# Optimization experiments

Hardware: AMD Instinct MI355X
Metric: run time of the kernel (lower is better)

## Reference

```python
import jax, jax.numpy as jnp
import numpy as np

B, M, K, N = 4, 2048, 4096, 4096


def setup_inputs() -> dict:
    key = jax.random.key(0)
    k1, k2, k3, k4, k5 = jax.random.split(key, 5)
    # quantized activations in [-8, 7], stored as int8 (spec dtype int32, cast here)
    x_q = jax.random.randint(k1, (B, M, K), -8, 8, dtype=jnp.int32).astype(jnp.int8)
    # per-token activation scales (B, M, 1)
    scales_x = jax.random.uniform(k2, (B, M, 1), dtype=jnp.float32, minval=0.001, maxval=0.02)
    # int8 weight (N, K) in [-8, 7] as produced by from_float
    weight = jax.random.randint(k3, (N, K), -8, 8, dtype=jnp.int32).astype(jnp.int8)
    # per-output-row weight scales (N, 1)
    weight_scales = jax.random.uniform(k4, (N, 1), dtype=jnp.float32, minval=0.001, maxval=0.02)
    bias = jax.random.normal(k5, (N,), dtype=jnp.float32) * 0.02
    return {"x_q": x_q, "scales_x": scales_x, "weight": weight,
            "weight_scales": weight_scales, "bias": bias}


def reference(x_q, scales_x, weight, weight_scales, bias):
    acc = jnp.einsum('bmk,nk->bmn', x_q, weight,
                     preferred_element_type=jnp.int32)  # (B, M, N) int32
    # sym_dequant: per-token scale * per-row weight scale, then fused bias add
    out = acc.astype(jnp.float32) * scales_x * weight_scales.reshape(1, 1, N) + bias
    return out
```

## Files before the change

kernel.cpp:

```cpp
#include <hip/hip_runtime.h>
#include <stdint.h>

#define MROWS 8192
#define K_DIM 4096
#define N_DIM 4096
#define BM 128
#define BN 128
#define BK 64

#define X_ELEMS (MROWS * K_DIM)
#define W_ELEMS (N_DIM * K_DIM)

typedef __attribute__((ext_vector_type(4))) int int4v;

#define GLOAD_LDS16(gptr, lptr)                                                   \
    __builtin_amdgcn_global_load_lds((const __attribute__((address_space(1))) void*)(gptr), \
                                     (__attribute__((address_space(3))) void*)(lptr), 16, 0, 0)

__device__ __forceinline__ int pack4(int4v v) {
    return (int)((unsigned)(v[0] & 0xFF)
               | ((unsigned)(v[1] & 0xFF) << 8)
               | ((unsigned)(v[2] & 0xFF) << 16)
               | ((unsigned)(v[3] & 0xFF) << 24));
}

__global__ __launch_bounds__(256) void pack_i32_to_i8(
    const int4v* __restrict__ src, int4v* __restrict__ dst, int n16)
{
    int i = blockIdx.x * blockDim.x + threadIdx.x;
    if (i >= n16) return;
    int4v a = src[4 * i + 0];
    int4v b = src[4 * i + 1];
    int4v c = src[4 * i + 2];
    int4v d = src[4 * i + 3];
    int4v r;
    r[0] = pack4(a); r[1] = pack4(b); r[2] = pack4(c); r[3] = pack4(d);
    dst[i] = r;
}

__global__ __launch_bounds__(256) void i8gemm_dq_kernel(
    const int8_t* __restrict__ xq,
    const float*  __restrict__ sx,
    const int8_t* __restrict__ wt,
    const float*  __restrict__ ws,
    const float*  __restrict__ bias,
    float*        __restrict__ out)
{
    __shared__ __align__(16) int8_t lsA[BM * BK];
    __shared__ __align__(16) int8_t lsB[BN * BK];

    const int tid  = threadIdx.x;
    const int wave = tid >> 6;
    const int lane = tid & 63;

    const int ct = blockIdx.x & 31;
    const int rt = blockIdx.x >> 5;

    const int wr = wave >> 1;
    const int wc = wave & 1;

    const int srow = wave * 16 + (lane >> 2);
    const int scol = (((lane & 3) - ((lane >> 3) & 3)) & 3) * 16;
    const int8_t* gA = xq + (size_t)(rt * BM + srow) * K_DIM + scol;
    const int8_t* gB = wt + (size_t)(ct * BN + srow) * K_DIM + scol;
    int8_t* lA = lsA + wave * 1024;
    int8_t* lB = lsB + wave * 1024;

    const int mrow = lane & 15;
    const int kswz = ((((lane >> 4) + (mrow >> 1)) & 3)) * 16;

    int4v acc[4][4] = {};

    const int kIters = K_DIM / BK;
    for (int kt = 0; kt < kIters; ++kt) {
        GLOAD_LDS16(gA,              lA);
        GLOAD_LDS16(gA + 64 * K_DIM, lA + 4096);
        GLOAD_LDS16(gB,              lB);
        GLOAD_LDS16(gB + 64 * K_DIM, lB + 4096);
        gA += BK;
        gB += BK;
        __syncthreads();

        int4v afrag[4], bfrag[4];
        #pragma unroll
        for (int i = 0; i < 4; ++i)
            afrag[i] = *(const int4v*)(lsA + (wr * 64 + i * 16 + mrow) * BK + kswz);
        #pragma unroll
        for (int j = 0; j < 4; ++j)
            bfrag[j] = *(const int4v*)(lsB + (wc * 64 + j * 16 + mrow) * BK + kswz);

        #pragma unroll
        for (int i = 0; i < 4; ++i)
            #pragma unroll
            for (int j = 0; j < 4; ++j)
                acc[i][j] = __builtin_amdgcn_mfma_i32_16x16x64_i8(
                                afrag[i], bfrag[j], acc[i][j], 0, 0, 0);

        __syncthreads();
    }

    const int row_base = rt * BM + wr * 64;
    const int col_base = ct * BN + wc * 64;
    const int crow = (lane >> 4) * 4;
    const int ccol = lane & 15;

    float wsc[4], bsc[4];
    #pragma unroll
    for (int j = 0; j < 4; ++j) {
        const int c = col_base + j * 16 + ccol;
        wsc[j] = ws[c];
        bsc[j] = bias[c];
    }

    #pragma unroll
    for (int i = 0; i < 4; ++i) {
        const int r0 = row_base + i * 16 + crow;
        float sx4[4];
        #pragma unroll
        for (int r = 0; r < 4; ++r) sx4[r] = sx[r0 + r];
        #pragma unroll
        for (int j = 0; j < 4; ++j) {
            const int c = col_base + j * 16 + ccol;
            float* o = out + (size_t)r0 * N_DIM + c;
            #pragma unroll
            for (int r = 0; r < 4; ++r)
                o[(size_t)r * N_DIM] = (float)acc[i][j][r] * sx4[r] * wsc[j] + bsc[j];
        }
    }
}

extern "C" void kernel_launch(void* const* d_in, const int* in_sizes, int n_in,
                              void* d_out, int out_size, void* d_ws, size_t ws_size,
                              hipStream_t stream) {
    const int*   xq32 = (const int*)d_in[0];
    const float* sx   = (const float*)d_in[1];
    const int*   wt32 = (const int*)d_in[2];
    const float* ws   = (const float*)d_in[3];
    const float* bias = (const float*)d_in[4];
    float* out = (float*)d_out;

    int8_t* xq8 = (int8_t*)d_ws;
    int8_t* wt8 = xq8 + (size_t)X_ELEMS;

    {
        int n16x = X_ELEMS / 16;
        int n16w = W_ELEMS / 16;
        pack_i32_to_i8<<<n16x / 256, 256, 0, stream>>>((const int4v*)xq32, (int4v*)xq8, n16x);
        pack_i32_to_i8<<<n16w / 256, 256, 0, stream>>>((const int4v*)wt32, (int4v*)wt8, n16w);
    }

    dim3 grid((MROWS / BM) * (N_DIM / BN));
    i8gemm_dq_kernel<<<grid, 256, 0, stream>>>(xq8, sx, wt8, ws, bias, out);
}
```

Before: 421.7 us.

## Enlarge GEMM tile to 256x256 with 4-stage LDS pipeline and 8 waves

Grows the block tile to 256x256 with 512 threads, and adds a 4-buffer LDS ring. Global-to-LDS loads for stage t+3 are issued between the MFMA groups, and each iteration needs only a single barrier. Blocks are remapped in a swizzle for L2 locality, and the pack kernel is simplified to one int per thread. The aim is to hide memory latency and raise compute intensity, at the cost of 128KB of LDS and higher register pressure from the 8x4 accumulators.

```diff
diff --git a/kernel.cpp b/kernel.cpp
--- a/kernel.cpp
+++ b/kernel.cpp
@@ -4,14 +4,18 @@
 #define MROWS 8192
 #define K_DIM 4096
 #define N_DIM 4096
-#define BM 128
-#define BN 128
+#define BM 256
+#define BN 256
 #define BK 64
+#define KT (K_DIM / BK)
+#define ABYTES (BM * BK)
+#define TBYTES (2 * ABYTES)
 
 #define X_ELEMS (MROWS * K_DIM)
 #define W_ELEMS (N_DIM * K_DIM)
 
-typedef __attribute__((ext_vector_type(4))) int int4v;
+typedef __attribute__((ext_vector_type(4))) int   int4v;
+typedef __attribute__((ext_vector_type(4))) float float4v;
 
 #define GLOAD_LDS16(gptr, lptr)                                                   \
     __builtin_amdgcn_global_load_lds((const __attribute__((address_space(1))) void*)(gptr), \
@@ -25,20 +29,13 @@
 }
 
 __global__ __launch_bounds__(256) void pack_i32_to_i8(
-    const int4v* __restrict__ src, int4v* __restrict__ dst, int n16)
+    const int4v* __restrict__ src, int* __restrict__ dst, int n4)
 {
     int i = blockIdx.x * blockDim.x + threadIdx.x;
-    if (i >= n16) return;
-    int4v a = src[4 * i + 0];
-    int4v b = src[4 * i + 1];
-    int4v c = src[4 * i + 2];
-    int4v d = src[4 * i + 3];
-    int4v r;
-    r[0] = pack4(a); r[1] = pack4(b); r[2] = pack4(c); r[3] = pack4(d);
-    dst[i] = r;
+    if (i < n4) dst[i] = pack4(src[i]);
 }
 
-__global__ __launch_bounds__(256) void i8gemm_dq_kernel(
+__global__ __launch_bounds__(512, 2) void i8gemm_dq_kernel(
     const int8_t* __restrict__ xq,
     const float*  __restrict__ sx,
     const int8_t* __restrict__ wt,
@@ -46,61 +43,95 @@
     const float*  __restrict__ bias,
     float*        __restrict__ out)
 {
-    __shared__ __align__(16) int8_t lsA[BM * BK];
-    __shared__ __align__(16) int8_t lsB[BN * BK];
+    __shared__ __align__(16) int8_t lds8[4 * TBYTES];
 
     const int tid  = threadIdx.x;
     const int wave = tid >> 6;
     const int lane = tid & 63;
+    const int wr   = wave >> 2;
+    const int wcn  = wave & 3;
 
-    const int ct = blockIdx.x & 31;
-    const int rt = blockIdx.x >> 5;
-
-    const int wr = wave >> 1;
-    const int wc = wave & 1;
+    const int bid = blockIdx.x;
+    const int wg  = (bid & 7) * 64 + (bid >> 3);
+    const int ct  = wg & 15;
+    const int rt  = wg >> 4;
 
     const int srow = wave * 16 + (lane >> 2);
     const int scol = (((lane & 3) - ((lane >> 3) & 3)) & 3) * 16;
-    const int8_t* gA = xq + (size_t)(rt * BM + srow) * K_DIM + scol;
-    const int8_t* gB = wt + (size_t)(ct * BN + srow) * K_DIM + scol;
-    int8_t* lA = lsA + wave * 1024;
-    int8_t* lB = lsB + wave * 1024;
+    const int8_t* gA0 = xq + (size_t)(rt * BM + srow) * K_DIM + scol;
+    const int8_t* gA1 = gA0 + (size_t)128 * K_DIM;
+    const int8_t* gB0 = wt + (size_t)(ct * BN + srow) * K_DIM + scol;
+    const int8_t* gB1 = gB0 + (size_t)128 * K_DIM;
+    const int dA0 = wave * 1024;
+    const int dA1 = 8192 + wave * 1024;
+    const int dB0 = ABYTES + wave * 1024;
+    const int dB1 = ABYTES + 8192 + wave * 1024;
 
     const int mrow = lane & 15;
-    const int kswz = ((((lane >> 4) + (mrow >> 1)) & 3)) * 16;
+    const int kswz = (((lane >> 4) + (mrow >> 1)) & 3) * 16;
+    const int aoff = (wr * 128 + mrow) * BK + kswz;
+    const int boff = ABYTES + (wcn * 64 + mrow) * BK + kswz;
 
-    int4v acc[4][4] = {};
+    int4v acc[8][4] = {};
 
-    const int kIters = K_DIM / BK;
-    for (int kt = 0; kt < kIters; ++kt) {
-        GLOAD_LDS16(gA,              lA);
-        GLOAD_LDS16(gA + 64 * K_DIM, lA + 4096);
-        GLOAD_LDS16(gB,              lB);
-        GLOAD_LDS16(gB + 64 * K_DIM, lB + 4096);
-        gA += BK;
-        gB += BK;
-        __syncthreads();
+    #pragma unroll
+    for (int u = 0; u < 3; ++u) {
+        const size_t ko = (size_t)u * BK;
+        int8_t* bb = lds8 + u * TBYTES;
+        GLOAD_LDS16(gA0 + ko, bb + dA0);
+        GLOAD_LDS16(gA1 + ko, bb + dA1);
+        GLOAD_LDS16(gB0 + ko, bb + dB0);
+        GLOAD_LDS16(gB1 + ko, bb + dB1);
+    }
 
-        int4v afrag[4], bfrag[4];
+    #pragma unroll 4
+    for (int t = 0; t < KT; ++t) {
+        const int  buf = t & 3;
+        const int  nb  = (t + 3) & 3;
+        const int  u   = (t + 3) & (KT - 1);
+        const size_t ko = (size_t)u * BK;
+        const int8_t* base = lds8 + buf * TBYTES;
+        int8_t* nbb = lds8 + nb * TBYTES;
+
+        asm volatile("s_waitcnt vmcnt(8)" ::: "memory");
+        __builtin_amdgcn_s_barrier();
+        __builtin_amdgcn_sched_barrier(0);
+
+        int4v a[4], b[4];
         #pragma unroll
-        for (int i = 0; i < 4; ++i)
-            afrag[i] = *(const int4v*)(lsA + (wr * 64 + i * 16 + mrow) * BK + kswz);
+        for (int i = 0; i < 4; ++i) a[i] = *(const int4v*)(base + aoff + i * 1024);
         #pragma unroll
-        for (int j = 0; j < 4; ++j)
-            bfrag[j] = *(const int4v*)(lsB + (wc * 64 + j * 16 + mrow) * BK + kswz);
+        for (int j = 0; j < 4; ++j) b[j] = *(const int4v*)(base + boff + j * 1024);
+        GLOAD_LDS16(gA0 + ko, nbb + dA0);
+        GLOAD_LDS16(gA1 + ko, nbb + dA1);
 
+        __builtin_amdgcn_s_setprio(1);
         #pragma unroll
         for (int i = 0; i < 4; ++i)
             #pragma unroll
             for (int j = 0; j < 4; ++j)
-                acc[i][j] = __builtin_amdgcn_mfma_i32_16x16x64_i8(
-                                afrag[i], bfrag[j], acc[i][j], 0, 0, 0);
+                acc[i][j] = __builtin_amdgcn_mfma_i32_16x16x64_i8(a[i], b[j], acc[i][j], 0, 0, 0);
+        __builtin_amdgcn_s_setprio(0);
 
-        __syncthreads();
+        int4v a2[4];
+        #pragma unroll
+        for (int i = 0; i < 4; ++i) a2[i] = *(const int4v*)(base + aoff + (4 + i) * 1024);
+        GLOAD_LDS16(gB0 + ko, nbb + dB0);
+        GLOAD_LDS16(gB1 + ko, nbb + dB1);
+
+        __builtin_amdgcn_s_setprio(1);
+        #pragma unroll
+        for (int i = 0; i < 4; ++i)
+            #pragma unroll
+            for (int j = 0; j < 4; ++j)
+                acc[4 + i][j] = __builtin_amdgcn_mfma_i32_16x16x64_i8(a2[i], b[j], acc[4 + i][j], 0, 0, 0);
+        __builtin_amdgcn_s_setprio(0);
     }
 
-    const int row_base = rt * BM + wr * 64;
-    const int col_base = ct * BN + wc * 64;
+    asm volatile("s_waitcnt vmcnt(0)" ::: "memory");
+
+    const int row_base = rt * BM + wr * 128;
+    const int col_base = ct * BN + wcn * 64;
     const int crow = (lane >> 4) * 4;
     const int ccol = lane & 15;
 
@@ -113,11 +144,9 @@
     }
 
     #pragma unroll
-    for (int i = 0; i < 4; ++i) {
+    for (int i = 0; i < 8; ++i) {
         const int r0 = row_base + i * 16 + crow;
-        float sx4[4];
-        #pragma unroll
-        for (int r = 0; r < 4; ++r) sx4[r] = sx[r0 + r];
+        const float4v sx4 = *(const float4v*)(sx + r0);
         #pragma unroll
         for (int j = 0; j < 4; ++j) {
             const int c = col_base + j * 16 + ccol;
@@ -143,12 +172,12 @@
     int8_t* wt8 = xq8 + (size_t)X_ELEMS;
 
     {
-        int n16x = X_ELEMS / 16;
-        int n16w = W_ELEMS / 16;
-        pack_i32_to_i8<<<n16x / 256, 256, 0, stream>>>((const int4v*)xq32, (int4v*)xq8, n16x);
-        pack_i32_to_i8<<<n16w / 256, 256, 0, stream>>>((const int4v*)wt32, (int4v*)wt8, n16w);
+        int n4x = X_ELEMS / 4;
+        int n4w = W_ELEMS / 4;
+        pack_i32_to_i8<<<n4x / 256, 256, 0, stream>>>((const int4v*)xq32, (int*)xq8, n4x);
+        pack_i32_to_i8<<<n4w / 256, 256, 0, stream>>>((const int4v*)wt32, (int*)wt8, n4w);
     }
 
     dim3 grid((MROWS / BM) * (N_DIM / BN));
-    i8gemm_dq_kernel<<<grid, 256, 0, stream>>>(xq8, sx, wt8, ws, bias, out);
+    i8gemm_dq_kernel<<<grid, 512, 0, stream>>>(xq8, sx, wt8, ws, bias, out);
 }
```

Result: faster. 388.5 us (-7.9%).
